# Optimization experiments

Hardware: AMD Instinct MI355X
Metric: run time of the kernel (lower is better)

The kernel has to match this reference:

```python
import jax, jax.numpy as jnp
import numpy as np

EPS = 1e-5  # torch BatchNorm1d default eps
B, IND, HID, OUT = 16384, 768, 4096, 10


@jax.custom_vjp
def ste_sign(x):
    # Binarize: sign(x) with 0 -> +1 (matches torch .data binarize + straight-through grad)
    return jnp.where(x >= 0, 1.0, -1.0).astype(x.dtype)

def _ste_fwd(x):
    return ste_sign(x), None

def _ste_bwd(_, g):
    return (g,)

ste_sign.defvjp(_ste_fwd, _ste_bwd)


def bn_eval(x, gamma, beta, mean, var):
    # eval-mode BatchNorm1d with running statistics
    return (x - mean) * (gamma * jax.lax.rsqrt(var + EPS)) + beta


def setup_inputs() -> dict:
    key = jax.random.key(0)
    ks = jax.random.split(key, 16)
    d = {"x": jax.random.normal(ks[0], (B, 784), jnp.float32)}
    dims = [(IND, HID), (HID, HID), (HID, HID), (HID, OUT)]
    for i, (fi, fo) in enumerate(dims, start=1):
        d[f"w{i}"] = jax.random.normal(ks[i], (fo, fi), jnp.float32) * 0.02
        d[f"b{i}"] = jnp.zeros((fo,), jnp.float32)
        d[f"g{i}"] = jnp.ones((fo,), jnp.float32)
        d[f"be{i}"] = jnp.zeros((fo,), jnp.float32)
        d[f"m{i}"] = jax.random.normal(ks[4 + i], (fo,), jnp.float32) * 0.1
        d[f"v{i}"] = jax.random.uniform(ks[8 + i], (fo,), jnp.float32, minval=0.5, maxval=1.5)
    return d


def reference(x, w1, b1, g1, be1, m1, v1,
              w2, b2, g2, be2, m2, v2,
              w3, b3, g3, be3, m3, v3,
              w4, b4, g4, be4, m4, v4):
    h = x.reshape(-1, 784)[:, :IND]            # [B, 768]
    # BinarizeLinear: sign(input) @ sign(W)^T + b  (first layer input size 768 != 784 -> binarized)
    h = ste_sign(h) @ ste_sign(w1).T + b1      # [B, HID]
    h = bn_eval(h, g1, be1, m1, v1)
    # self.htanh*(x) in the original is never assigned -> no-op, omitted
    h = ste_sign(h) @ ste_sign(w2).T + b2
    h = bn_eval(h, g2, be2, m2, v2)
    h = ste_sign(h) @ ste_sign(w3).T + b3
    h = bn_eval(h, g3, be3, m3, v3)
    h = ste_sign(h) @ ste_sign(w4).T + b4      # [B, 10]
    h = bn_eval(h, g4, be4, m4, v4)
    return jax.nn.log_softmax(h, axis=1)
```

## Files before the change

### kernel.cpp

```cpp
#include <hip/hip_runtime.h>
#include <stdint.h>

typedef unsigned long long u64;
typedef int v4i  __attribute__((ext_vector_type(4)));
typedef int v8i  __attribute__((ext_vector_type(8)));
typedef float v16f __attribute__((ext_vector_type(16)));

#define BATCH 16384
#define IND   768
#define HID   4096
#define NOUT  10
#define EPS   1e-5f

__device__ __forceinline__ unsigned nib8(unsigned b) {
    unsigned e = ((b & 0x55u) * 0x00208208u) & 0x08080808u;
    unsigned o = (((b >> 1) & 0x55u) * 0x00208208u) & 0x08080808u;
    return 0x22222222u | e | (o << 4);
}

__device__ __forceinline__ void gload16(const v4i* g, v4i* l) {
    __builtin_amdgcn_global_load_lds(
        (const __attribute__((address_space(1))) void*)g,
        (__attribute__((address_space(3))) void*)l, 16, 0, 0);
}

__global__ void pack_sign_kernel(const float* __restrict__ src, int ld, int nwords,
                                 int nrows, u64* __restrict__ dst) {
    int gt   = blockIdx.x * blockDim.x + threadIdx.x;
    int wave = gt >> 6;
    int lane = gt & 63;
    if (wave >= nrows) return;
    const float* row = src + (size_t)wave * ld;
    u64* drow = dst + (size_t)wave * nwords;
    for (int w = 0; w < nwords; ++w) {
        float v = row[(w << 6) + lane];
        u64 m = __ballot(v < 0.0f);
        if (lane == 0) drow[w] = m;
    }
}

__global__ void pack_nib_t_kernel(const float* __restrict__ src, int ld,
                                  int nwords, int nrows, unsigned* __restrict__ dst) {
    int row  = blockIdx.x;
    int wave = threadIdx.x >> 6, lane = threadIdx.x & 63;
    int nw4  = (nwords + 3) >> 2;
    int wend = (wave + 1) * nw4; if (wend > nwords) wend = nwords;
    const float* r = src + (size_t)row * ld;
    for (int w = wave * nw4; w < wend; ++w) {
        u64 m = __ballot(r[(w << 6) + lane] < 0.0f);
        if (lane < 8) {
            unsigned d = nib8((unsigned)(m >> (8 * lane)) & 0xFFu);
            dst[((size_t)(2 * w + (lane >> 2)) * nrows + row) * 4 + (lane & 3)] = d;
        }
    }
}

__global__ void expand_bits_kernel(const u64* __restrict__ src,
                                   v4i* __restrict__ dst) {
    int t = blockIdx.x * blockDim.x + threadIdx.x;
    if (t >= 64 * BATCH) return;
    int w = t >> 14, r = t & (BATCH - 1);
    u64 m = src[((size_t)w << 14) + r];
    v4i o0, o1;
    #pragma unroll
    for (int d = 0; d < 4; ++d) {
        o0[d] = (int)nib8((unsigned)(m >> (8 * d)) & 0xFFu);
        o1[d] = (int)nib8((unsigned)(m >> (32 + 8 * d)) & 0xFFu);
    }
    dst[((size_t)(2 * w) << 14) + r]     = o0;
    dst[((size_t)(2 * w + 1) << 14) + r] = o1;
}

__global__ __launch_bounds__(512, 2) void bgemm_fp4s(
    const v4i* __restrict__ AN,
    int rounds,
    const v4i* __restrict__ WN,
    const float* __restrict__ bias, const float* __restrict__ gam,
    const float* __restrict__ bet,  const float* __restrict__ mu,
    const float* __restrict__ var,
    unsigned* __restrict__ ONIB,
    u64* __restrict__ OT,
    u64* __restrict__ ORM)
{
    __shared__ v4i sb[2][4][256];

    const int bm = blockIdx.x >> 4, bn = blockIdx.x & 15;
    const int m0 = bm << 8, n0 = bn << 8;
    const int tid = threadIdx.x;
    const int wave = tid >> 6, lane = tid & 63;
    const int wm = wave >> 2, wn = wave & 3;
    const int l31 = lane & 31, q = lane >> 5;

    v16f acc[4][2];
    #pragma unroll
    for (int a = 0; a < 4; ++a)
        #pragma unroll
        for (int b = 0; b < 2; ++b)
            #pragma unroll
            for (int k = 0; k < 16; ++k) acc[a][b][k] = 0.0f;

    const int spl = wave >> 1, sr0 = (wave & 1) << 7;
    const v4i* gpA = AN + (size_t)spl * BATCH + (m0 + sr0 + lane);
    const size_t cstepA = (size_t)4 * BATCH;

    const v4i* gpW = WN + (size_t)q * HID + (n0 + (wn << 6) + l31);
    const size_t cstepW = (size_t)4 * HID;

    union F { v8i v; v4i h[2]; };
    const v4i z4 = {0, 0, 0, 0};
    const int sc1 = 0x7f7f7f7f;

    gload16(gpA,      &sb[0][spl][sr0]);
    gload16(gpA + 64, &sb[0][spl][sr0 + 64]);
    v4i rw[4], nw[4];
    #pragma unroll
    for (int k4 = 0; k4 < 4; ++k4) {
        rw[k4] = gpW[(size_t)(2 * (k4 >> 1)) * HID + 32 * (k4 & 1)];
        nw[k4] = z4;
    }
    gpA += cstepA; gpW += cstepW;
    __syncthreads();

    int buf = 0;
    for (int c = 0; c < rounds; ++c) {
        if (c + 1 < rounds) {
            gload16(gpA,      &sb[buf ^ 1][spl][sr0]);
            gload16(gpA + 64, &sb[buf ^ 1][spl][sr0 + 64]);
            #pragma unroll
            for (int k4 = 0; k4 < 4; ++k4)
                nw[k4] = gpW[(size_t)(2 * (k4 >> 1)) * HID + 32 * (k4 & 1)];
            gpA += cstepA; gpW += cstepW;
        }
        #pragma unroll
        for (int ks = 0; ks < 2; ++ks) {
            const int pl = 2 * ks + q;
            v4i a4[4];
            #pragma unroll
            for (int ti = 0; ti < 4; ++ti)
                a4[ti] = sb[buf][pl][(wm << 7) + (ti << 5) + l31];
            #pragma unroll
            for (int ti = 0; ti < 4; ++ti) {
                F fa; fa.h[0] = a4[ti]; fa.h[1] = z4;
                #pragma unroll
                for (int tj = 0; tj < 2; ++tj) {
                    F fb; fb.h[0] = rw[2 * ks + tj]; fb.h[1] = z4;
                    acc[ti][tj] = __builtin_amdgcn_mfma_scale_f32_32x32x64_f8f6f4(
                        fa.v, fb.v, acc[ti][tj], 4, 4, 0, sc1, 0, sc1);
                }
            }
        }
        __syncthreads();
        #pragma unroll
        for (int k4 = 0; k4 < 4; ++k4) rw[k4] = nw[k4];
        buf ^= 1;
    }

    float scj[2], muj[2], bej[2], bij[2];
    #pragma unroll
    for (int tj = 0; tj < 2; ++tj) {
        int col = n0 + (wn << 6) + 32 * tj + l31;
        scj[tj] = gam[col] * rsqrtf(var[col] + EPS);
        muj[tj] = mu[col]; bej[tj] = bet[col]; bij[tj] = bias[col];
    }
    const int pbase = (n0 + (wn << 6)) >> 5;
    const int pn    = (n0 + (wn << 6)) >> 6;

    #pragma unroll
    for (int ti = 0; ti < 4; ++ti) {
        #pragma unroll
        for (int reg = 0; reg < 16; ++reg) {
            int rbase = (reg & 3) + 8 * (reg >> 2);
            int rA = m0 + (wm << 7) + (ti << 5) + rbase;
            u64 bl[2];
            #pragma unroll
            for (int tj = 0; tj < 2; ++tj) {
                float h = acc[ti][tj][reg] + bij[tj];
                float y = (h - muj[tj]) * scj[tj] + bej[tj];
                bl[tj] = __ballot(y < 0.0f);
            }
            u64 wA = (bl[0] & 0xFFFFFFFFull) | (bl[1] << 32);
            u64 wB = (bl[0] >> 32) | (bl[1] & 0xFFFFFFFF00000000ull);
            if (ONIB && lane < 16) {
                u64 src = (lane < 8) ? wA : wB;
                int row = rA + ((lane < 8) ? 0 : 4);
                int j   = lane & 7;
                unsigned byte = (unsigned)(src >> (8 * j)) & 0xFFu;
                ONIB[((size_t)(pbase + (j >> 2)) * BATCH + row) * 4 + (j & 3)]
                    = nib8(byte);
            }
            if (OT && lane == 0) {
                OT[(size_t)pn * BATCH + rA]     = wA;
                OT[(size_t)pn * BATCH + rA + 4] = wB;
            }
            if (ORM && lane == 0) {
                ORM[(size_t)rA * 64 + pn]       = wA;
                ORM[(size_t)(rA + 4) * 64 + pn] = wB;
            }
        }
    }
}

__global__ void final_layer_kernel(
    const u64* __restrict__ Ap,
    const u64* __restrict__ Wp,
    const float* __restrict__ bias, const float* __restrict__ gam,
    const float* __restrict__ bet,  const float* __restrict__ mu,
    const float* __restrict__ var,
    float* __restrict__ out)
{
    int gt   = blockIdx.x * blockDim.x + threadIdx.x;
    int row  = gt >> 6;
    int lane = gt & 63;
    if (row >= BATCH) return;

    u64 a = Ap[(size_t)row * 64 + lane];
    unsigned p[NOUT];
    #pragma unroll
    for (int j = 0; j < NOUT; ++j)
        p[j] = (unsigned)__popcll(a ^ Wp[j * 64 + lane]);

    #pragma unroll
    for (int j = 0; j < NOUT; ++j) {
        #pragma unroll
        for (int off = 32; off >= 1; off >>= 1)
            p[j] += __shfl_xor(p[j], off, 64);
    }

    float z[NOUT];
    float mx = -1e30f;
    #pragma unroll
    for (int j = 0; j < NOUT; ++j) {
        float hh = (float)(HID - 2 * (int)p[j]) + bias[j];
        float sc = gam[j] * rsqrtf(var[j] + EPS);
        z[j] = (hh - mu[j]) * sc + bet[j];
        mx = fmaxf(mx, z[j]);
    }
    float s = 0.0f;
    #pragma unroll
    for (int j = 0; j < NOUT; ++j) s += expf(z[j] - mx);
    float lse = logf(s) + mx;
    if (lane < NOUT) out[(size_t)row * NOUT + lane] = z[lane] - lse;
}

extern "C" void kernel_launch(void* const* d_in, const int* in_sizes, int n_in,
                              void* d_out, int out_size, void* d_ws, size_t ws_size,
                              hipStream_t stream) {
    (void)in_sizes; (void)n_in; (void)out_size; (void)ws_size;

    const float* x   = (const float*)d_in[0];
    const float* w1  = (const float*)d_in[1];
    const float* b1  = (const float*)d_in[2];
    const float* g1  = (const float*)d_in[3];
    const float* be1 = (const float*)d_in[4];
    const float* m1  = (const float*)d_in[5];
    const float* v1  = (const float*)d_in[6];
    const float* w2  = (const float*)d_in[7];
    const float* b2  = (const float*)d_in[8];
    const float* g2  = (const float*)d_in[9];
    const float* be2 = (const float*)d_in[10];
    const float* m2  = (const float*)d_in[11];
    const float* v2  = (const float*)d_in[12];
    const float* w3  = (const float*)d_in[13];
    const float* b3  = (const float*)d_in[14];
    const float* g3  = (const float*)d_in[15];
    const float* be3 = (const float*)d_in[16];
    const float* m3  = (const float*)d_in[17];
    const float* v3  = (const float*)d_in[18];
    const float* w4  = (const float*)d_in[19];
    const float* b4  = (const float*)d_in[20];
    const float* g4  = (const float*)d_in[21];
    const float* be4 = (const float*)d_in[22];
    const float* m4  = (const float*)d_in[23];
    const float* v4  = (const float*)d_in[24];

    char* ws = (char*)d_ws;
    unsigned* XN    = (unsigned*)(ws);
    unsigned* W1N   = (unsigned*)(ws + 6291456);
    unsigned* WBN   = (unsigned*)(ws + 7864320);
    unsigned* ANa   = (unsigned*)(ws + 16252928);
    u64*      aBits = (u64*)     (ws + 49807360);
    u64*      a3RM  = (u64*)     (ws + 58195968);
    u64*      w4p   = (u64*)     (ws + 66584576);

    pack_nib_t_kernel<<<BATCH, 256, 0, stream>>>(x, 784, 12, BATCH, XN);
    pack_nib_t_kernel<<<HID, 256, 0, stream>>>(w1, IND, 12, HID, W1N);
    pack_nib_t_kernel<<<HID, 256, 0, stream>>>(w2, HID, 64, HID, WBN);
    pack_sign_kernel<<<3, 256, 0, stream>>>(w4, HID, 64, NOUT, w4p);

    bgemm_fp4s<<<1024, 512, 0, stream>>>((const v4i*)XN, 6, (const v4i*)W1N,
                                         b1, g1, be1, m1, v1,
                                         ANa, nullptr, nullptr);
    bgemm_fp4s<<<1024, 512, 0, stream>>>((const v4i*)ANa, 32, (const v4i*)WBN,
                                         b2, g2, be2, m2, v2,
                                         nullptr, aBits, nullptr);
    pack_nib_t_kernel<<<HID, 256, 0, stream>>>(w3, HID, 64, HID, WBN);
    expand_bits_kernel<<<4096, 256, 0, stream>>>(aBits, (v4i*)ANa);

    bgemm_fp4s<<<1024, 512, 0, stream>>>((const v4i*)ANa, 32, (const v4i*)WBN,
                                         b3, g3, be3, m3, v3,
                                         nullptr, nullptr, a3RM);

    final_layer_kernel<<<BATCH / 4, 256, 0, stream>>>(a3RM, w4p,
                                                      b4, g4, be4, m4, v4,
                                                      (float*)d_out);
}
```

Measured before the change: 719.0 us.

## Triple-buffer LDS A tiles with one barrier per k-step and inline-asm reads

Measured after the change: 707.1 us. About the same (-1.7%).

```diff
diff --git a/kernel.cpp b/kernel.cpp
--- a/kernel.cpp
+++ b/kernel.cpp
@@ -71,7 +71,70 @@
     dst[((size_t)(2 * w + 1) << 14) + r] = o1;
 }
 
-__global__ __launch_bounds__(512, 2) void bgemm_fp4s(
+__device__ __forceinline__ void kstep(
+    int c, int rounds,
+    const v4i*& gpA, const v4i*& gpW,
+    unsigned& stOff, unsigned& rdOff,
+    char* ldsBase, int sOff, unsigned rdBase,
+    v4i* rwU, v4i* rwL,
+    v16f acc[4][2])
+{
+    const v4i z4 = {0, 0, 0, 0};
+    const int sc1 = 0x7f7f7f7f;
+
+    asm volatile("s_waitcnt vmcnt(6)" ::: "memory");
+    __builtin_amdgcn_s_barrier();
+    __builtin_amdgcn_sched_barrier(0);
+
+    if (c + 2 < rounds) {
+        gload16(gpA,      (v4i*)(ldsBase + stOff + sOff));
+        gload16(gpA + 64, (v4i*)(ldsBase + stOff + sOff + 1024));
+        gpA += (size_t)4 * BATCH;
+    }
+    if (c + 1 < rounds) {
+        #pragma unroll
+        for (int k4 = 0; k4 < 4; ++k4)
+            rwL[k4] = gpW[(size_t)(2 * (k4 >> 1)) * HID + 32 * (k4 & 1)];
+        gpW += (size_t)4 * HID;
+    }
+
+    v4i af0, af1, af2, af3, af4, af5, af6, af7;
+    unsigned ra = rdBase + rdOff;
+    asm volatile(
+        "ds_read_b128 %0, %8 offset:0\n\t"
+        "ds_read_b128 %1, %8 offset:512\n\t"
+        "ds_read_b128 %2, %8 offset:1024\n\t"
+        "ds_read_b128 %3, %8 offset:1536\n\t"
+        "ds_read_b128 %4, %8 offset:8192\n\t"
+        "ds_read_b128 %5, %8 offset:8704\n\t"
+        "ds_read_b128 %6, %8 offset:9216\n\t"
+        "ds_read_b128 %7, %8 offset:9728"
+        : "=&v"(af0), "=&v"(af1), "=&v"(af2), "=&v"(af3),
+          "=&v"(af4), "=&v"(af5), "=&v"(af6), "=&v"(af7)
+        : "v"(ra));
+    asm volatile("s_waitcnt lgkmcnt(0)" ::: "memory");
+    __builtin_amdgcn_sched_barrier(0);
+
+    union F { v8i v; v4i h[2]; };
+    v4i afs[8] = {af0, af1, af2, af3, af4, af5, af6, af7};
+    #pragma unroll
+    for (int ks = 0; ks < 2; ++ks) {
+        #pragma unroll
+        for (int ti = 0; ti < 4; ++ti) {
+            F fa; fa.h[0] = afs[ks * 4 + ti]; fa.h[1] = z4;
+            #pragma unroll
+            for (int tj = 0; tj < 2; ++tj) {
+                F fb; fb.h[0] = rwU[2 * ks + tj]; fb.h[1] = z4;
+                acc[ti][tj] = __builtin_amdgcn_mfma_scale_f32_32x32x64_f8f6f4(
+                    fa.v, fb.v, acc[ti][tj], 4, 4, 0, sc1, 0, sc1);
+            }
+        }
+    }
+    stOff = (stOff == 32768u) ? 0u : stOff + 16384u;
+    rdOff = (rdOff == 32768u) ? 0u : rdOff + 16384u;
+}
+
+__global__ __launch_bounds__(512, 2) void bgemm_fp4p(
     const v4i* __restrict__ AN,
     int rounds,
     const v4i* __restrict__ WN,
@@ -82,7 +145,7 @@
     u64* __restrict__ OT,
     u64* __restrict__ ORM)
 {
-    __shared__ v4i sb[2][4][256];
+    __shared__ v4i sb[3][4][256];
 
     const int bm = blockIdx.x >> 4, bn = blockIdx.x & 15;
     const int m0 = bm << 8, n0 = bn << 8;
@@ -101,58 +164,30 @@
 
     const int spl = wave >> 1, sr0 = (wave & 1) << 7;
     const v4i* gpA = AN + (size_t)spl * BATCH + (m0 + sr0 + lane);
-    const size_t cstepA = (size_t)4 * BATCH;
-
     const v4i* gpW = WN + (size_t)q * HID + (n0 + (wn << 6) + l31);
-    const size_t cstepW = (size_t)4 * HID;
-
-    union F { v8i v; v4i h[2]; };
-    const v4i z4 = {0, 0, 0, 0};
-    const int sc1 = 0x7f7f7f7f;
-
-    gload16(gpA,      &sb[0][spl][sr0]);
-    gload16(gpA + 64, &sb[0][spl][sr0 + 64]);
-    v4i rw[4], nw[4];
-    #pragma unroll
-    for (int k4 = 0; k4 < 4; ++k4) {
-        rw[k4] = gpW[(size_t)(2 * (k4 >> 1)) * HID + 32 * (k4 & 1)];
-        nw[k4] = z4;
-    }
-    gpA += cstepA; gpW += cstepW;
-    __syncthreads();
-
-    int buf = 0;
-    for (int c = 0; c < rounds; ++c) {
-        if (c + 1 < rounds) {
-            gload16(gpA,      &sb[buf ^ 1][spl][sr0]);
-            gload16(gpA + 64, &sb[buf ^ 1][spl][sr0 + 64]);
-            #pragma unroll
-            for (int k4 = 0; k4 < 4; ++k4)
-                nw[k4] = gpW[(size_t)(2 * (k4 >> 1)) * HID + 32 * (k4 & 1)];
-            gpA += cstepA; gpW += cstepW;
-        }
-        #pragma unroll
-        for (int ks = 0; ks < 2; ++ks) {
-            const int pl = 2 * ks + q;
-            v4i a4[4];
-            #pragma unroll
-            for (int ti = 0; ti < 4; ++ti)
-                a4[ti] = sb[buf][pl][(wm << 7) + (ti << 5) + l31];
-            #pragma unroll
-            for (int ti = 0; ti < 4; ++ti) {
-                F fa; fa.h[0] = a4[ti]; fa.h[1] = z4;
-                #pragma unroll
-                for (int tj = 0; tj < 2; ++tj) {
-                    F fb; fb.h[0] = rw[2 * ks + tj]; fb.h[1] = z4;
-                    acc[ti][tj] = __builtin_amdgcn_mfma_scale_f32_32x32x64_f8f6f4(
-                        fa.v, fb.v, acc[ti][tj], 4, 4, 0, sc1, 0, sc1);
-                }
-            }
-        }
-        __syncthreads();
-        #pragma unroll
-        for (int k4 = 0; k4 < 4; ++k4) rw[k4] = nw[k4];
-        buf ^= 1;
+
+    char* ldsBase = (char*)&sb[0][0][0];
+    const int sOff = spl * 4096 + (sr0 << 4);
+    unsigned rdBase = (unsigned)(q * 4096 + (((wm << 7) + l31) << 4));
+
+    gload16(gpA,      (v4i*)(ldsBase + sOff));
+    gload16(gpA + 64, (v4i*)(ldsBase + sOff + 1024));
+    gpA += (size_t)4 * BATCH;
+    gload16(gpA,      (v4i*)(ldsBase + 16384 + sOff));
+    gload16(gpA + 64, (v4i*)(ldsBase + 16384 + sOff + 1024));
+    gpA += (size_t)4 * BATCH;
+    v4i rwA[4], rwB[4];
+    #pragma unroll
+    for (int k4 = 0; k4 < 4; ++k4)
+        rwA[k4] = gpW[(size_t)(2 * (k4 >> 1)) * HID + 32 * (k4 & 1)];
+    gpW += (size_t)4 * HID;
+
+    unsigned stOff = 32768u, rdOff = 0u;
+    for (int c = 0; c < rounds; c += 2) {
+        kstep(c,     rounds, gpA, gpW, stOff, rdOff, ldsBase, sOff, rdBase,
+              rwA, rwB, acc);
+        kstep(c + 1, rounds, gpA, gpW, stOff, rdOff, ldsBase, sOff, rdBase,
+              rwB, rwA, acc);
     }
 
     float scj[2], muj[2], bej[2], bij[2];
@@ -287,16 +322,16 @@
     pack_nib_t_kernel<<<HID, 256, 0, stream>>>(w2, HID, 64, HID, WBN);
     pack_sign_kernel<<<3, 256, 0, stream>>>(w4, HID, 64, NOUT, w4p);
 
-    bgemm_fp4s<<<1024, 512, 0, stream>>>((const v4i*)XN, 6, (const v4i*)W1N,
+    bgemm_fp4p<<<1024, 512, 0, stream>>>((const v4i*)XN, 6, (const v4i*)W1N,
                                          b1, g1, be1, m1, v1,
                                          ANa, nullptr, nullptr);
-    bgemm_fp4s<<<1024, 512, 0, stream>>>((const v4i*)ANa, 32, (const v4i*)WBN,
+    bgemm_fp4p<<<1024, 512, 0, stream>>>((const v4i*)ANa, 32, (const v4i*)WBN,
                                          b2, g2, be2, m2, v2,
                                          nullptr, aBits, nullptr);
     pack_nib_t_kernel<<<HID, 256, 0, stream>>>(w3, HID, 64, HID, WBN);
     expand_bits_kernel<<<4096, 256, 0, stream>>>(aBits, (v4i*)ANa);
 
-    bgemm_fp4s<<<1024, 512, 0, stream>>>((const v4i*)ANa, 32, (const v4i*)WBN,
+    bgemm_fp4p<<<1024, 512, 0, stream>>>((const v4i*)ANa, 32, (const v4i*)WBN,
                                          b3, g3, be3, m3, v3,
                                          nullptr, nullptr, a3RM);
 
```

## Triple-buffer A and W tiles in LDS with interleaved async loads and inline ds_reads

Applied to the files above, without the earlier changes.

Measured after the change: 690.8 us. 3.9% less time.

```diff
diff --git a/kernel.cpp b/kernel.cpp
--- a/kernel.cpp
+++ b/kernel.cpp
@@ -18,7 +18,7 @@
     return 0x22222222u | e | (o << 4);
 }
 
-__device__ __forceinline__ void gload16(const v4i* g, v4i* l) {
+__device__ __forceinline__ void gload16(const v4i* g, char* l) {
     __builtin_amdgcn_global_load_lds(
         (const __attribute__((address_space(1))) void*)g,
         (__attribute__((address_space(3))) void*)l, 16, 0, 0);
@@ -71,7 +71,7 @@
     dst[((size_t)(2 * w + 1) << 14) + r] = o1;
 }
 
-__global__ __launch_bounds__(512, 2) void bgemm_fp4s(
+__global__ __launch_bounds__(512, 2) void bgemm_fp4q(
     const v4i* __restrict__ AN,
     int rounds,
     const v4i* __restrict__ WN,
@@ -82,7 +82,8 @@
     u64* __restrict__ OT,
     u64* __restrict__ ORM)
 {
-    __shared__ v4i sb[2][4][256];
+    __shared__ v4i sbuf[6144];
+    char* lds = (char*)sbuf;
 
     const int bm = blockIdx.x >> 4, bn = blockIdx.x & 15;
     const int m0 = bm << 8, n0 = bn << 8;
@@ -99,60 +100,108 @@
             #pragma unroll
             for (int k = 0; k < 16; ++k) acc[a][b][k] = 0.0f;
 
-    const int spl = wave >> 1, sr0 = (wave & 1) << 7;
-    const v4i* gpA = AN + (size_t)spl * BATCH + (m0 + sr0 + lane);
-    const size_t cstepA = (size_t)4 * BATCH;
-
-    const v4i* gpW = WN + (size_t)q * HID + (n0 + (wn << 6) + l31);
-    const size_t cstepW = (size_t)4 * HID;
+    const v4i* pA1 = AN + (size_t)(tid >> 8) * BATCH + (m0 + (tid & 255));
+    const v4i* pA2 = pA1 + 2 * BATCH;
+    const v4i* pW1 = WN + (size_t)(tid >> 8) * HID + (n0 + (tid & 255));
+    const v4i* pW2 = pW1 + 2 * HID;
+    const unsigned dA1 = (unsigned)(tid << 4);
+    const unsigned dA2 = dA1 + 8192u;
+    const unsigned dW1 = dA1 + 16384u;
+    const unsigned dW2 = dA1 + 24576u;
+
+    const unsigned rdA = (unsigned)(q * 4096 + (((wm << 7) + l31) << 4));
+    const unsigned rdW = (unsigned)(16384 + q * 4096 + (((wn << 6) + l31) << 4));
 
     union F { v8i v; v4i h[2]; };
     const v4i z4 = {0, 0, 0, 0};
     const int sc1 = 0x7f7f7f7f;
 
-    gload16(gpA,      &sb[0][spl][sr0]);
-    gload16(gpA + 64, &sb[0][spl][sr0 + 64]);
-    v4i rw[4], nw[4];
-    #pragma unroll
-    for (int k4 = 0; k4 < 4; ++k4) {
-        rw[k4] = gpW[(size_t)(2 * (k4 >> 1)) * HID + 32 * (k4 & 1)];
-        nw[k4] = z4;
-    }
-    gpA += cstepA; gpW += cstepW;
-    __syncthreads();
-
-    int buf = 0;
+    #pragma unroll
+    for (int t2 = 0; t2 < 2; ++t2) {
+        unsigned b = (unsigned)t2 * 32768u;
+        gload16(pA1, lds + b + dA1); pA1 += 4 * BATCH;
+        gload16(pA2, lds + b + dA2); pA2 += 4 * BATCH;
+        gload16(pW1, lds + b + dW1); pW1 += 4 * HID;
+        gload16(pW2, lds + b + dW2); pW2 += 4 * HID;
+    }
+    unsigned rdBuf = 0u, stBuf = 65536u;
+
+    v4i fa0, fa1, fw00, fw01, fw10, fw11;
+
     for (int c = 0; c < rounds; ++c) {
-        if (c + 1 < rounds) {
-            gload16(gpA,      &sb[buf ^ 1][spl][sr0]);
-            gload16(gpA + 64, &sb[buf ^ 1][spl][sr0 + 64]);
-            #pragma unroll
-            for (int k4 = 0; k4 < 4; ++k4)
-                nw[k4] = gpW[(size_t)(2 * (k4 >> 1)) * HID + 32 * (k4 & 1)];
-            gpA += cstepA; gpW += cstepW;
+        const bool st = (c + 2 < rounds);
+        if (st) { asm volatile("s_waitcnt vmcnt(4)" ::: "memory"); }
+        else    { asm volatile("s_waitcnt vmcnt(0)" ::: "memory"); }
+        __builtin_amdgcn_s_barrier();
+        unsigned aA = rdA + rdBuf;
+        unsigned aW = rdW + rdBuf;
+        asm volatile("ds_read_b128 %0, %2 offset:0\n\t"
+                     "ds_read_b128 %1, %2 offset:8192"
+                     : "=&v"(fa0), "=&v"(fa1) : "v"(aA));
+        asm volatile("ds_read_b128 %0, %4 offset:0\n\t"
+                     "ds_read_b128 %1, %4 offset:512\n\t"
+                     "ds_read_b128 %2, %4 offset:8192\n\t"
+                     "ds_read_b128 %3, %4 offset:8704"
+                     : "=&v"(fw00), "=&v"(fw01), "=&v"(fw10), "=&v"(fw11)
+                     : "v"(aW));
+        if (st) { gload16(pA1, lds + stBuf + dA1); pA1 += 4 * BATCH; }
+        asm volatile("s_waitcnt lgkmcnt(0)" ::: "memory");
+        __builtin_amdgcn_sched_barrier(0);
+        __builtin_amdgcn_s_setprio(1);
+        {
+            F a0; a0.h[0] = fa0; a0.h[1] = z4;
+            F a1; a1.h[0] = fa1; a1.h[1] = z4;
+            F b00; b00.h[0] = fw00; b00.h[1] = z4;
+            F b01; b01.h[0] = fw01; b01.h[1] = z4;
+            F b10; b10.h[0] = fw10; b10.h[1] = z4;
+            F b11; b11.h[0] = fw11; b11.h[1] = z4;
+            acc[0][0] = __builtin_amdgcn_mfma_scale_f32_32x32x64_f8f6f4(
+                a0.v, b00.v, acc[0][0], 4, 4, 0, sc1, 0, sc1);
+            acc[0][1] = __builtin_amdgcn_mfma_scale_f32_32x32x64_f8f6f4(
+                a0.v, b01.v, acc[0][1], 4, 4, 0, sc1, 0, sc1);
+            acc[0][0] = __builtin_amdgcn_mfma_scale_f32_32x32x64_f8f6f4(
+                a1.v, b10.v, acc[0][0], 4, 4, 0, sc1, 0, sc1);
+            acc[0][1] = __builtin_amdgcn_mfma_scale_f32_32x32x64_f8f6f4(
+                a1.v, b11.v, acc[0][1], 4, 4, 0, sc1, 0, sc1);
         }
+        __builtin_amdgcn_s_setprio(0);
+        __builtin_amdgcn_s_barrier();
         #pragma unroll
-        for (int ks = 0; ks < 2; ++ks) {
-            const int pl = 2 * ks + q;
-            v4i a4[4];
-            #pragma unroll
-            for (int ti = 0; ti < 4; ++ti)
-                a4[ti] = sb[buf][pl][(wm << 7) + (ti << 5) + l31];
-            #pragma unroll
-            for (int ti = 0; ti < 4; ++ti) {
-                F fa; fa.h[0] = a4[ti]; fa.h[1] = z4;
-                #pragma unroll
-                for (int tj = 0; tj < 2; ++tj) {
-                    F fb; fb.h[0] = rw[2 * ks + tj]; fb.h[1] = z4;
-                    acc[ti][tj] = __builtin_amdgcn_mfma_scale_f32_32x32x64_f8f6f4(
-                        fa.v, fb.v, acc[ti][tj], 4, 4, 0, sc1, 0, sc1);
-                }
-            }
+        for (int p = 1; p < 4; ++p) {
+            unsigned aAp = aA + (unsigned)(p * 512);
+            asm volatile("ds_read_b128 %0, %2 offset:0\n\t"
+                         "ds_read_b128 %1, %2 offset:8192"
+                         : "=&v"(fa0), "=&v"(fa1) : "v"(aAp));
+            if (st) {
+                if (p == 1) { gload16(pA2, lds + stBuf + dA2); pA2 += 4 * BATCH; }
+                if (p == 2) { gload16(pW1, lds + stBuf + dW1); pW1 += 4 * HID; }
+                if (p == 3) { gload16(pW2, lds + stBuf + dW2); pW2 += 4 * HID; }
+            }
+            __builtin_amdgcn_s_barrier();
+            asm volatile("s_waitcnt lgkmcnt(0)" ::: "memory");
+            __builtin_amdgcn_sched_barrier(0);
+            __builtin_amdgcn_s_setprio(1);
+            {
+                F a0; a0.h[0] = fa0; a0.h[1] = z4;
+                F a1; a1.h[0] = fa1; a1.h[1] = z4;
+                F b00; b00.h[0] = fw00; b00.h[1] = z4;
+                F b01; b01.h[0] = fw01; b01.h[1] = z4;
+                F b10; b10.h[0] = fw10; b10.h[1] = z4;
+                F b11; b11.h[0] = fw11; b11.h[1] = z4;
+                acc[p][0] = __builtin_amdgcn_mfma_scale_f32_32x32x64_f8f6f4(
+                    a0.v, b00.v, acc[p][0], 4, 4, 0, sc1, 0, sc1);
+                acc[p][1] = __builtin_amdgcn_mfma_scale_f32_32x32x64_f8f6f4(
+                    a0.v, b01.v, acc[p][1], 4, 4, 0, sc1, 0, sc1);
+                acc[p][0] = __builtin_amdgcn_mfma_scale_f32_32x32x64_f8f6f4(
+                    a1.v, b10.v, acc[p][0], 4, 4, 0, sc1, 0, sc1);
+                acc[p][1] = __builtin_amdgcn_mfma_scale_f32_32x32x64_f8f6f4(
+                    a1.v, b11.v, acc[p][1], 4, 4, 0, sc1, 0, sc1);
+            }
+            __builtin_amdgcn_s_setprio(0);
+            __builtin_amdgcn_s_barrier();
         }
-        __syncthreads();
-        #pragma unroll
-        for (int k4 = 0; k4 < 4; ++k4) rw[k4] = nw[k4];
-        buf ^= 1;
+        rdBuf = (rdBuf == 65536u) ? 0u : rdBuf + 32768u;
+        stBuf = (stBuf == 65536u) ? 0u : stBuf + 32768u;
     }
 
     float scj[2], muj[2], bej[2], bij[2];
@@ -287,16 +336,16 @@
     pack_nib_t_kernel<<<HID, 256, 0, stream>>>(w2, HID, 64, HID, WBN);
     pack_sign_kernel<<<3, 256, 0, stream>>>(w4, HID, 64, NOUT, w4p);
 
-    bgemm_fp4s<<<1024, 512, 0, stream>>>((const v4i*)XN, 6, (const v4i*)W1N,
+    bgemm_fp4q<<<1024, 512, 0, stream>>>((const v4i*)XN, 6, (const v4i*)W1N,
                                          b1, g1, be1, m1, v1,
                                          ANa, nullptr, nullptr);
-    bgemm_fp4s<<<1024, 512, 0, stream>>>((const v4i*)ANa, 32, (const v4i*)WBN,
+    bgemm_fp4q<<<1024, 512, 0, stream>>>((const v4i*)ANa, 32, (const v4i*)WBN,
                                          b2, g2, be2, m2, v2,
                                          nullptr, aBits, nullptr);
     pack_nib_t_kernel<<<HID, 256, 0, stream>>>(w3, HID, 64, HID, WBN);
     expand_bits_kernel<<<4096, 256, 0, stream>>>(aBits, (v4i*)ANa);
 
-    bgemm_fp4s<<<1024, 512, 0, stream>>>((const v4i*)ANa, 32, (const v4i*)WBN,
+    bgemm_fp4q<<<1024, 512, 0, stream>>>((const v4i*)ANa, 32, (const v4i*)WBN,
                                          b3, g3, be3, m3, v3,
                                          nullptr, nullptr, a3RM);
 
```
